# Performance work log

Measured on AMD Instinct MI355X. Metric: run time of the kernel, lower is better.

## Reference

```python
import jax, jax.numpy as jnp
import numpy as np

N_NODES = 50000
N_EDGES = 800000
NFEAT, NHID, NCLASS = 512, 256, 64


def spmm(src, dst, w, h):
    """Sparse adj @ dense h via gather + segment_sum.
    out[i] = sum over edges e with dst[e]==i of w[e] * h[src[e]]."""
    msgs = h[src] * w[:, None]  # [E, d]
    return jax.ops.segment_sum(msgs, dst, num_segments=N_NODES)


def setup_inputs() -> dict:
    key = jax.random.key(0)
    ks = jax.random.split(key, 10)
    return {
        "x": jax.random.normal(ks[0], (N_NODES, NFEAT), dtype=jnp.float32),
        "edge_src0": jax.random.randint(ks[1], (N_EDGES,), 0, N_NODES),
        "edge_dst0": jax.random.randint(ks[2], (N_EDGES,), 0, N_NODES),
        "edge_w0": jax.random.uniform(ks[3], (N_EDGES,), dtype=jnp.float32),
        "edge_src1": jax.random.randint(ks[4], (N_EDGES,), 0, N_NODES),
        "edge_dst1": jax.random.randint(ks[5], (N_EDGES,), 0, N_NODES),
        "edge_w1": jax.random.uniform(ks[6], (N_EDGES,), dtype=jnp.float32),
        "W1": jax.random.normal(ks[7], (NFEAT, NHID), dtype=jnp.float32) * (1.0 / np.sqrt(NFEAT)),
        "b1": jnp.zeros((NHID,), dtype=jnp.float32),
        "W2": jax.random.normal(ks[8], (NHID, NCLASS), dtype=jnp.float32) * (1.0 / np.sqrt(NHID)),
        "b2": jnp.zeros((NCLASS,), dtype=jnp.float32),
    }


def reference(x, edge_src0, edge_dst0, edge_w0, edge_src1, edge_dst1, edge_w1, W1, b1, W2, b2):
    # Layer 1: GCN conv (skip=False) + ReLU. Dropout is identity in eval mode.
    h = jax.nn.relu(spmm(edge_src0, edge_dst0, edge_w0, x @ W1) + b1)
    # Layer 2: GCN conv (skip=False)
    logits = spmm(edge_src1, edge_dst1, edge_w1, h @ W2) + b2
    return jax.nn.log_softmax(logits, axis=1)
```

## Files before the change

### kernel.cpp

```cpp
#include <hip/hip_runtime.h>

#define N_NODES 50000
#define N_EDGES 800000
#define NFEAT   512
#define NHID    256
#define NCLASS  64

#define MTILES     ((N_NODES + 63) / 64)

#define NBUCK      196
#define BCAP       5632
#define BIN_CHUNK  4096
#define BIN_BLOCKS ((N_EDGES + BIN_CHUNK - 1) / BIN_CHUNK)

typedef short short8  __attribute__((ext_vector_type(8)));
typedef float floatx4 __attribute__((ext_vector_type(4)));

__device__ inline short f2bf(float f) {
    unsigned u = __builtin_bit_cast(unsigned, f);
    u += 0x7FFF + ((u >> 16) & 1);
    return (short)(u >> 16);
}
__device__ inline float bf2f(short v) {
    unsigned u = ((unsigned)(unsigned short)v) << 16;
    return __builtin_bit_cast(float, u);
}
__device__ inline int pack_edge(int src, float w) {
    return (src & 0xFFFF) | ((int)(unsigned short)f2bf(w) << 16);
}

__global__ __launch_bounds__(256) void cast_w1t_kernel(const float* __restrict__ W1,
                                                       short* __restrict__ Wt) {
    const int k = blockIdx.x;
    const int n = threadIdx.x;
    Wt[n * NFEAT + k] = f2bf(W1[k * NHID + n]);
}

__global__ __launch_bounds__(256) void cast_w2t_kernel(const float* __restrict__ W2,
                                                       short* __restrict__ W2t) {
    const int n = blockIdx.x;
    const int k = threadIdx.x;
    W2t[n * NHID + k] = f2bf(W2[k * NCLASS + n]);
}

__global__ __launch_bounds__(256) void binscatter_kernel(
    const int* __restrict__ es0, const int* __restrict__ ed0, const float* __restrict__ ew0,
    int* __restrict__ cur0, int2* __restrict__ bin0,
    const int* __restrict__ es1, const int* __restrict__ ed1, const float* __restrict__ ew1,
    int* __restrict__ cur1, int2* __restrict__ bin1) {
    __shared__ int hist[NBUCK];
    const int list = blockIdx.x >= BIN_BLOCKS;
    const int cb   = blockIdx.x - list * BIN_BLOCKS;
    const int*   es  = list ? es1 : es0;
    const int*   ed  = list ? ed1 : ed0;
    const float* ew  = list ? ew1 : ew0;
    int*         cur = list ? cur1 : cur0;
    int2*        bin = list ? bin1 : bin0;

    const int e0 = cb * BIN_CHUNK;
    const int e1 = min(e0 + BIN_CHUNK, N_EDGES);
    const int t  = threadIdx.x;

    if (t < NBUCK) hist[t] = 0;
    __syncthreads();
    for (int e = e0 + t; e < e1; e += 256)
        atomicAdd(&hist[ed[e] >> 8], 1);
    __syncthreads();
    if (t < NBUCK) hist[t] = atomicAdd(&cur[t], hist[t]);
    __syncthreads();
    for (int e = e0 + t; e < e1; e += 256) {
        int d = ed[e];
        int b = d >> 8;
        int p = atomicAdd(&hist[b], 1);
        if (p < BCAP) {
            int2 v; v.x = pack_edge(es[e], ew[e]); v.y = d;
            bin[(size_t)b * BCAP + p] = v;
        }
    }
}

__global__ __launch_bounds__(256) void bucket_scan_kernel(const int* __restrict__ cur0, int* __restrict__ bb0,
                                                          const int* __restrict__ cur1, int* __restrict__ bb1) {
    __shared__ int s[256];
    const int* cur = blockIdx.x ? cur1 : cur0;
    int*       bb  = blockIdx.x ? bb1  : bb0;
    int t = threadIdx.x;
    int v = (t < NBUCK) ? min(cur[t], BCAP) : 0;
    s[t] = v;
    __syncthreads();
    for (int off = 1; off < 256; off <<= 1) {
        int a = (t >= off) ? s[t - off] : 0;
        __syncthreads();
        s[t] += a;
        __syncthreads();
    }
    if (t < NBUCK) bb[t] = s[t] - v;
}

__global__ __launch_bounds__(256) void bucket_csr_kernel(
    const int* __restrict__ cur0, const int* __restrict__ bb0, const int2* __restrict__ bin0,
    int* __restrict__ deg0, int* __restrict__ base0, int* __restrict__ edge0,
    const int* __restrict__ cur1, const int* __restrict__ bb1, const int2* __restrict__ bin1,
    int* __restrict__ deg1, int* __restrict__ base1, int* __restrict__ edge1) {
    __shared__ int dh[256];
    __shared__ int sc[256];
    const int list = blockIdx.x >= NBUCK;
    const int b    = blockIdx.x - list * NBUCK;
    const int*  cur  = list ? cur1  : cur0;
    const int*  bb   = list ? bb1   : bb0;
    const int2* bin  = (list ? bin1 : bin0) + (size_t)b * BCAP;
    int*        deg  = list ? deg1  : deg0;
    int*        base = list ? base1 : base0;
    int*        edge = list ? edge1 : edge0;

    const int len   = min(cur[b], BCAP);
    const int gbase = bb[b];
    const int n0    = b << 8;
    const int t     = threadIdx.x;

    dh[t] = 0;
    __syncthreads();
    for (int i = t; i < len; i += 256)
        atomicAdd(&dh[bin[i].y & 255], 1);
    __syncthreads();
    int v = dh[t];
    sc[t] = v;
    __syncthreads();
    for (int off = 1; off < 256; off <<= 1) {
        int a = (t >= off) ? sc[t - off] : 0;
        __syncthreads();
        sc[t] += a;
        __syncthreads();
    }
    int excl = sc[t] - v;
    int node = n0 + t;
    if (node < N_NODES) { deg[node] = v; base[node] = gbase + excl; }
    dh[t] = gbase + excl;
    __syncthreads();
    for (int i = t; i < len; i += 256) {
        int2 ev = bin[i];
        int p = atomicAdd(&dh[ev.y & 255], 1);
        edge[p] = ev.x;
    }
}

__global__ __launch_bounds__(256) void gemm1_mfma_kernel(const float* __restrict__ x,
                                                         const short* __restrict__ Wt,
                                                         short* __restrict__ h0b) {
    __shared__ short As[64 * 32];
    __shared__ short Bs[256 * 32];
    const int tid  = threadIdx.x;
    const int wave = tid >> 6, lane = tid & 63;
    const int mlo  = lane & 15, q = lane >> 4;
    const int m0   = blockIdx.x * 64;

    const int ar  = tid >> 2;
    const int acg = (tid & 3) * 8;
    int arow = m0 + ar; if (arow >= N_NODES) arow = N_NODES - 1;
    const float* aptr = x + (size_t)arow * NFEAT + acg;

    floatx4 acc[4][4] = {};

    for (int kc = 0; kc < NFEAT; kc += 32) {
        float4 a0 = *(const float4*)(aptr + kc);
        float4 a1 = *(const float4*)(aptr + kc + 4);
        short8 ap;
        ap[0]=f2bf(a0.x); ap[1]=f2bf(a0.y); ap[2]=f2bf(a0.z); ap[3]=f2bf(a0.w);
        ap[4]=f2bf(a1.x); ap[5]=f2bf(a1.y); ap[6]=f2bf(a1.z); ap[7]=f2bf(a1.w);
        *(short8*)&As[ar * 32 + acg] = ap;
        #pragma unroll
        for (int it = 0; it < 4; ++it) {
            int g = it * 256 + tid;
            *(short8*)&Bs[g * 8] =
                *(const short8*)(Wt + (size_t)(g >> 2) * NFEAT + kc + (g & 3) * 8);
        }
        __syncthreads();

        short8 af[4], bfr[4];
        #pragma unroll
        for (int t = 0; t < 4; ++t)
            af[t] = *(const short8*)&As[(t * 16 + mlo) * 32 + q * 8];
        #pragma unroll
        for (int u = 0; u < 4; ++u)
            bfr[u] = *(const short8*)&Bs[(wave * 64 + u * 16 + mlo) * 32 + q * 8];
        #pragma unroll
        for (int t = 0; t < 4; ++t)
            #pragma unroll
            for (int u = 0; u < 4; ++u)
                acc[t][u] = __builtin_amdgcn_mfma_f32_16x16x32_bf16(af[t], bfr[u], acc[t][u], 0, 0, 0);
        __syncthreads();
    }

    #pragma unroll
    for (int t = 0; t < 4; ++t) {
        #pragma unroll
        for (int r = 0; r < 4; ++r) {
            int row = m0 + t * 16 + q * 4 + r;
            if (row < N_NODES) {
                #pragma unroll
                for (int u = 0; u < 4; ++u)
                    h0b[(size_t)row * NHID + wave * 64 + u * 16 + mlo] = f2bf(acc[t][u][r]);
            }
        }
    }
}

__global__ __launch_bounds__(256) void spmm1_pull_kernel(const int* __restrict__ base,
                                                         const int* __restrict__ deg,
                                                         const int* __restrict__ edge_s,
                                                         const short* __restrict__ h0b,
                                                         float* __restrict__ agg0) {
    const int node = blockIdx.x * 4 + (threadIdx.x >> 6);
    const int lane = threadIdx.x & 63;
    const int slot = lane >> 5;
    const int c    = lane & 31;
    const int start = base[node];
    const int len   = deg[node];

    float acc[8] = {0.f,0.f,0.f,0.f,0.f,0.f,0.f,0.f};
    int j = slot;
    int e = 0;
    short8 hv = {0,0,0,0,0,0,0,0};
    if (j < len) {
        e  = edge_s[start + j];
        hv = *(const short8*)(h0b + (size_t)(e & 0xFFFF) * NHID + c * 8);
    }
    while (j < len) {
        float wt = bf2f((short)((unsigned)e >> 16));
        int jn = j + 2;
        int en = e; short8 hn = hv;
        if (jn < len) {
            en = edge_s[start + jn];
            hn = *(const short8*)(h0b + (size_t)(en & 0xFFFF) * NHID + c * 8);
        }
        #pragma unroll
        for (int k = 0; k < 8; ++k) acc[k] += wt * bf2f(hv[k]);
        e = en; hv = hn; j = jn;
    }
    #pragma unroll
    for (int k = 0; k < 8; ++k) acc[k] += __shfl_xor(acc[k], 32);
    if (slot == 0) {
        float4 o0 = {acc[0], acc[1], acc[2], acc[3]};
        float4 o1 = {acc[4], acc[5], acc[6], acc[7]};
        float* p = agg0 + (size_t)node * NHID + c * 8;
        *(float4*)p = o0;
        *(float4*)(p + 4) = o1;
    }
}

__global__ __launch_bounds__(256) void gemm2_mfma_kernel(const float* __restrict__ agg0,
                                                         const float* __restrict__ b1,
                                                         const short* __restrict__ W2t,
                                                         short* __restrict__ h2b) {
    __shared__ short Bs[64 * 264];
    __shared__ short As[64 * 32];
    const int tid  = threadIdx.x;
    const int wave = tid >> 6, lane = tid & 63;
    const int mlo  = lane & 15, q = lane >> 4;
    const int m0   = blockIdx.x * 64;

    {
        int n = tid >> 2, seg = (tid & 3) * 64;
        #pragma unroll
        for (int i = 0; i < 8; ++i)
            *(short8*)&Bs[n * 264 + seg + i * 8] =
                *(const short8*)(W2t + n * NHID + seg + i * 8);
    }

    const int ar  = tid >> 2;
    const int acg = (tid & 3) * 8;
    int arow = m0 + ar; if (arow >= N_NODES) arow = N_NODES - 1;
    const float* aptr = agg0 + (size_t)arow * NHID + acg;

    floatx4 acc[4] = {};

    for (int kc = 0; kc < NHID; kc += 32) {
        float4 a0 = *(const float4*)(aptr + kc);
        float4 a1 = *(const float4*)(aptr + kc + 4);
        float4 c0 = *(const float4*)(b1 + kc + acg);
        float4 c1 = *(const float4*)(b1 + kc + acg + 4);
        float v0 = a0.x + c0.x, v1 = a0.y + c0.y, v2 = a0.z + c0.z, v3 = a0.w + c0.w;
        float v4 = a1.x + c1.x, v5 = a1.y + c1.y, v6 = a1.z + c1.z, v7 = a1.w + c1.w;
        short8 apk;
        apk[0] = f2bf(v0 > 0.f ? v0 : 0.f); apk[1] = f2bf(v1 > 0.f ? v1 : 0.f);
        apk[2] = f2bf(v2 > 0.f ? v2 : 0.f); apk[3] = f2bf(v3 > 0.f ? v3 : 0.f);
        apk[4] = f2bf(v4 > 0.f ? v4 : 0.f); apk[5] = f2bf(v5 > 0.f ? v5 : 0.f);
        apk[6] = f2bf(v6 > 0.f ? v6 : 0.f); apk[7] = f2bf(v7 > 0.f ? v7 : 0.f);
        *(short8*)&As[ar * 32 + acg] = apk;
        __syncthreads();

        short8 af = *(const short8*)&As[(wave * 16 + mlo) * 32 + q * 8];
        #pragma unroll
        for (int u = 0; u < 4; ++u) {
            short8 bfr = *(const short8*)&Bs[(u * 16 + mlo) * 264 + kc + q * 8];
            acc[u] = __builtin_amdgcn_mfma_f32_16x16x32_bf16(af, bfr, acc[u], 0, 0, 0);
        }
        __syncthreads();
    }

    #pragma unroll
    for (int r = 0; r < 4; ++r) {
        int row = m0 + wave * 16 + q * 4 + r;
        if (row < N_NODES) {
            #pragma unroll
            for (int u = 0; u < 4; ++u)
                h2b[(size_t)row * NCLASS + u * 16 + mlo] = f2bf(acc[u][r]);
        }
    }
}

__global__ __launch_bounds__(256) void spmm2_lsm_kernel(const int* __restrict__ base,
                                                        const int* __restrict__ deg,
                                                        const int* __restrict__ edge_s,
                                                        const short* __restrict__ h2b,
                                                        const float* __restrict__ b2,
                                                        float* __restrict__ out) {
    const int node = blockIdx.x * 4 + (threadIdx.x >> 6);
    const int lane = threadIdx.x & 63;
    const int slot = lane >> 3;
    const int f    = lane & 7;
    const int start = base[node];
    const int len   = deg[node];

    float acc[8] = {0.f,0.f,0.f,0.f,0.f,0.f,0.f,0.f};
    int j = slot;
    int e = 0;
    short8 hv = {0,0,0,0,0,0,0,0};
    if (j < len) {
        e  = edge_s[start + j];
        hv = *(const short8*)(h2b + (size_t)(e & 0xFFFF) * NCLASS + f * 8);
    }
    while (j < len) {
        float wt = bf2f((short)((unsigned)e >> 16));
        int jn = j + 8;
        int en = e; short8 hn = hv;
        if (jn < len) {
            en = edge_s[start + jn];
            hn = *(const short8*)(h2b + (size_t)(en & 0xFFFF) * NCLASS + f * 8);
        }
        #pragma unroll
        for (int k = 0; k < 8; ++k) acc[k] += wt * bf2f(hv[k]);
        e = en; hv = hn; j = jn;
    }
    #pragma unroll
    for (int k = 0; k < 8; ++k) {
        acc[k] += __shfl_xor(acc[k], 8);
        acc[k] += __shfl_xor(acc[k], 16);
        acc[k] += __shfl_xor(acc[k], 32);
    }
    float4 c0 = *(const float4*)(b2 + f * 8);
    float4 c1 = *(const float4*)(b2 + f * 8 + 4);
    float v[8];
    v[0] = acc[0] + c0.x; v[1] = acc[1] + c0.y; v[2] = acc[2] + c0.z; v[3] = acc[3] + c0.w;
    v[4] = acc[4] + c1.x; v[5] = acc[5] + c1.y; v[6] = acc[6] + c1.z; v[7] = acc[7] + c1.w;
    float m = v[0];
    #pragma unroll
    for (int k = 1; k < 8; ++k) m = fmaxf(m, v[k]);
    m = fmaxf(m, __shfl_xor(m, 1));
    m = fmaxf(m, __shfl_xor(m, 2));
    m = fmaxf(m, __shfl_xor(m, 4));
    float s = 0.f;
    #pragma unroll
    for (int k = 0; k < 8; ++k) s += __expf(v[k] - m);
    s += __shfl_xor(s, 1);
    s += __shfl_xor(s, 2);
    s += __shfl_xor(s, 4);
    float ls = m + __logf(s);
    if (slot == 0) {
        float4 o0 = {v[0] - ls, v[1] - ls, v[2] - ls, v[3] - ls};
        float4 o1 = {v[4] - ls, v[5] - ls, v[6] - ls, v[7] - ls};
        float* p = out + (size_t)node * NCLASS + f * 8;
        *(float4*)p = o0;
        *(float4*)(p + 4) = o1;
    }
}

extern "C" void kernel_launch(void* const* d_in, const int* in_sizes, int n_in,
                              void* d_out, int out_size, void* d_ws, size_t ws_size,
                              hipStream_t stream) {
    const float* x   = (const float*)d_in[0];
    const int*   es0 = (const int*)  d_in[1];
    const int*   ed0 = (const int*)  d_in[2];
    const float* ew0 = (const float*)d_in[3];
    const int*   es1 = (const int*)  d_in[4];
    const int*   ed1 = (const int*)  d_in[5];
    const float* ew1 = (const float*)d_in[6];
    const float* W1  = (const float*)d_in[7];
    const float* b1  = (const float*)d_in[8];
    const float* W2  = (const float*)d_in[9];
    const float* b2  = (const float*)d_in[10];
    float* out = (float*)d_out;

    char* ws = (char*)d_ws;
    const size_t SZ_H0 = (size_t)N_NODES * NHID * sizeof(short);
    const size_t SZ_BIN = (size_t)NBUCK * BCAP * sizeof(int2);
    short* h0b  = (short*)ws;
    short* h2b  = (short*)ws;
    float* agg0 = (float*)(ws + (size_t)N_NODES * NHID * sizeof(float));

    int2* bin0 = (int2*)(ws + SZ_H0);
    int2* bin1 = (int2*)(ws + SZ_H0 + SZ_BIN);

    char* c1 = ws + 44000000;
    int* deg1  = (int*)c1;
    int* base1 = deg1 + N_NODES;
    int* edge1 = base1 + N_NODES;
    int* cur0  = edge1 + N_EDGES;
    int* cur1  = cur0 + 256;
    int* bb0   = cur1 + 256;
    int* bb1   = bb0 + 256;

    int*   deg0  = (int*)d_out;
    int*   base0 = deg0 + N_NODES;
    int*   edge0 = base0 + N_NODES;
    short* Wt    = (short*)((char*)d_out + (8u << 20));
    short* W2t   = (short*)((char*)d_out + (9u << 20));

    hipMemsetAsync(cur0, 0, 512 * sizeof(int), stream);
    binscatter_kernel<<<2 * BIN_BLOCKS, 256, 0, stream>>>(es0, ed0, ew0, cur0, bin0,
                                                          es1, ed1, ew1, cur1, bin1);
    bucket_scan_kernel<<<2, 256, 0, stream>>>(cur0, bb0, cur1, bb1);
    bucket_csr_kernel<<<2 * NBUCK, 256, 0, stream>>>(cur0, bb0, bin0, deg0, base0, edge0,
                                                     cur1, bb1, bin1, deg1, base1, edge1);

    cast_w1t_kernel<<<NFEAT, 256, 0, stream>>>(W1, Wt);
    cast_w2t_kernel<<<NCLASS, 256, 0, stream>>>(W2, W2t);

    gemm1_mfma_kernel<<<MTILES, 256, 0, stream>>>(x, Wt, h0b);
    spmm1_pull_kernel<<<N_NODES / 4, 256, 0, stream>>>(base0, deg0, edge0, h0b, agg0);

    gemm2_mfma_kernel<<<MTILES, 256, 0, stream>>>(agg0, b1, W2t, h2b);
    spmm2_lsm_kernel<<<N_NODES / 4, 256, 0, stream>>>(base1, deg1, edge1, h2b, b2, out);
}
```

Measured before the change: 362.1 us.

## Tile weight transposes via LDS and deepen GEMM K-tiles with swizzled LDS

New measurement: 354.9 us. 1.02x faster.

```diff
diff --git a/kernel.cpp b/kernel.cpp
--- a/kernel.cpp
+++ b/kernel.cpp
@@ -29,18 +29,67 @@
     return (src & 0xFFFF) | ((int)(unsigned short)f2bf(w) << 16);
 }
 
+typedef __attribute__((address_space(3))) void       lds_void;
+typedef __attribute__((address_space(1))) const void glb_void;
+__device__ inline void gload_lds16(const void* g, void* l) {
+    __builtin_amdgcn_global_load_lds((glb_void*)g, (lds_void*)l, 16, 0, 0);
+}
+
 __global__ __launch_bounds__(256) void cast_w1t_kernel(const float* __restrict__ W1,
                                                        short* __restrict__ Wt) {
-    const int k = blockIdx.x;
-    const int n = threadIdx.x;
-    Wt[n * NFEAT + k] = f2bf(W1[k * NHID + n]);
+    __shared__ short tile[64][72];
+    const int t  = threadIdx.x;
+    const int k0 = (blockIdx.x >> 2) << 6;
+    const int n0 = (blockIdx.x & 3) << 6;
+    {
+        int kr = t >> 2, ng = (t & 3) << 4;
+        const float* src = W1 + (size_t)(k0 + kr) * NHID + n0 + ng;
+        float4 v0 = ((const float4*)src)[0], v1 = ((const float4*)src)[1];
+        float4 v2 = ((const float4*)src)[2], v3 = ((const float4*)src)[3];
+        short* d = &tile[kr][ng];
+        d[0]=f2bf(v0.x); d[1]=f2bf(v0.y); d[2]=f2bf(v0.z); d[3]=f2bf(v0.w);
+        d[4]=f2bf(v1.x); d[5]=f2bf(v1.y); d[6]=f2bf(v1.z); d[7]=f2bf(v1.w);
+        d[8]=f2bf(v2.x); d[9]=f2bf(v2.y); d[10]=f2bf(v2.z); d[11]=f2bf(v2.w);
+        d[12]=f2bf(v3.x); d[13]=f2bf(v3.y); d[14]=f2bf(v3.z); d[15]=f2bf(v3.w);
+    }
+    __syncthreads();
+    {
+        int nr = t >> 2, kg = (t & 3) << 4;
+        short8 o0, o1;
+        #pragma unroll
+        for (int j = 0; j < 8; ++j) { o0[j] = tile[kg + j][nr]; o1[j] = tile[kg + 8 + j][nr]; }
+        short* d = Wt + (size_t)(n0 + nr) * NFEAT + k0 + kg;
+        *(short8*)d = o0;
+        *(short8*)(d + 8) = o1;
+    }
 }
 
 __global__ __launch_bounds__(256) void cast_w2t_kernel(const float* __restrict__ W2,
                                                        short* __restrict__ W2t) {
-    const int n = blockIdx.x;
-    const int k = threadIdx.x;
-    W2t[n * NHID + k] = f2bf(W2[k * NCLASS + n]);
+    __shared__ short tile[64][72];
+    const int t  = threadIdx.x;
+    const int k0 = blockIdx.x << 6;
+    {
+        int kr = t >> 2, ng = (t & 3) << 4;
+        const float* src = W2 + (size_t)(k0 + kr) * NCLASS + ng;
+        float4 v0 = ((const float4*)src)[0], v1 = ((const float4*)src)[1];
+        float4 v2 = ((const float4*)src)[2], v3 = ((const float4*)src)[3];
+        short* d = &tile[kr][ng];
+        d[0]=f2bf(v0.x); d[1]=f2bf(v0.y); d[2]=f2bf(v0.z); d[3]=f2bf(v0.w);
+        d[4]=f2bf(v1.x); d[5]=f2bf(v1.y); d[6]=f2bf(v1.z); d[7]=f2bf(v1.w);
+        d[8]=f2bf(v2.x); d[9]=f2bf(v2.y); d[10]=f2bf(v2.z); d[11]=f2bf(v2.w);
+        d[12]=f2bf(v3.x); d[13]=f2bf(v3.y); d[14]=f2bf(v3.z); d[15]=f2bf(v3.w);
+    }
+    __syncthreads();
+    {
+        int nr = t >> 2, kg = (t & 3) << 4;
+        short8 o0, o1;
+        #pragma unroll
+        for (int j = 0; j < 8; ++j) { o0[j] = tile[kg + j][nr]; o1[j] = tile[kg + 8 + j][nr]; }
+        short* d = W2t + (size_t)nr * NHID + k0 + kg;
+        *(short8*)d = o0;
+        *(short8*)(d + 8) = o1;
+    }
 }
 
 __global__ __launch_bounds__(256) void binscatter_kernel(
@@ -147,47 +196,63 @@
 __global__ __launch_bounds__(256) void gemm1_mfma_kernel(const float* __restrict__ x,
                                                          const short* __restrict__ Wt,
                                                          short* __restrict__ h0b) {
-    __shared__ short As[64 * 32];
-    __shared__ short Bs[256 * 32];
+    __shared__ short As[64 * 64];
+    __shared__ short Bs[256 * 64];
     const int tid  = threadIdx.x;
     const int wave = tid >> 6, lane = tid & 63;
     const int mlo  = lane & 15, q = lane >> 4;
     const int m0   = blockIdx.x * 64;
 
-    const int ar  = tid >> 2;
-    const int acg = (tid & 3) * 8;
+    const int ar = tid >> 2;
+    const int cp = (tid & 3) * 2;
     int arow = m0 + ar; if (arow >= N_NODES) arow = N_NODES - 1;
-    const float* aptr = x + (size_t)arow * NFEAT + acg;
+    const float* aptr = x + (size_t)arow * NFEAT + cp * 8;
+
+    const int brl = lane >> 3;
+    const int bsl = lane & 7;
 
     floatx4 acc[4][4] = {};
 
-    for (int kc = 0; kc < NFEAT; kc += 32) {
+    for (int kc = 0; kc < NFEAT; kc += 64) {
+        #pragma unroll
+        for (int i = 0; i < 8; ++i) {
+            int r  = wave * 64 + i * 8 + brl;
+            int sc2 = bsl ^ (r & 7);
+            gload_lds16(Wt + (size_t)r * NFEAT + kc + sc2 * 8,
+                        &Bs[(wave * 64 + i * 8) * 64]);
+        }
         float4 a0 = *(const float4*)(aptr + kc);
         float4 a1 = *(const float4*)(aptr + kc + 4);
-        short8 ap;
-        ap[0]=f2bf(a0.x); ap[1]=f2bf(a0.y); ap[2]=f2bf(a0.z); ap[3]=f2bf(a0.w);
-        ap[4]=f2bf(a1.x); ap[5]=f2bf(a1.y); ap[6]=f2bf(a1.z); ap[7]=f2bf(a1.w);
-        *(short8*)&As[ar * 32 + acg] = ap;
-        #pragma unroll
-        for (int it = 0; it < 4; ++it) {
-            int g = it * 256 + tid;
-            *(short8*)&Bs[g * 8] =
-                *(const short8*)(Wt + (size_t)(g >> 2) * NFEAT + kc + (g & 3) * 8);
-        }
-        __syncthreads();
-
-        short8 af[4], bfr[4];
-        #pragma unroll
-        for (int t = 0; t < 4; ++t)
-            af[t] = *(const short8*)&As[(t * 16 + mlo) * 32 + q * 8];
-        #pragma unroll
-        for (int u = 0; u < 4; ++u)
-            bfr[u] = *(const short8*)&Bs[(wave * 64 + u * 16 + mlo) * 32 + q * 8];
-        #pragma unroll
-        for (int t = 0; t < 4; ++t)
+        float4 a2 = *(const float4*)(aptr + kc + 8);
+        float4 a3 = *(const float4*)(aptr + kc + 12);
+        short8 p0, p1;
+        p0[0]=f2bf(a0.x); p0[1]=f2bf(a0.y); p0[2]=f2bf(a0.z); p0[3]=f2bf(a0.w);
+        p0[4]=f2bf(a1.x); p0[5]=f2bf(a1.y); p0[6]=f2bf(a1.z); p0[7]=f2bf(a1.w);
+        p1[0]=f2bf(a2.x); p1[1]=f2bf(a2.y); p1[2]=f2bf(a2.z); p1[3]=f2bf(a2.w);
+        p1[4]=f2bf(a3.x); p1[5]=f2bf(a3.y); p1[6]=f2bf(a3.z); p1[7]=f2bf(a3.w);
+        *(short8*)&As[ar * 64 + ((cp     ) ^ (ar & 7)) * 8] = p0;
+        *(short8*)&As[ar * 64 + ((cp + 1) ^ (ar & 7)) * 8] = p1;
+        __syncthreads();
+
+        #pragma unroll
+        for (int h = 0; h < 2; ++h) {
+            short8 afv[4], bfv[4];
             #pragma unroll
-            for (int u = 0; u < 4; ++u)
-                acc[t][u] = __builtin_amdgcn_mfma_f32_16x16x32_bf16(af[t], bfr[u], acc[t][u], 0, 0, 0);
+            for (int t = 0; t < 4; ++t) {
+                int r = t * 16 + mlo;
+                afv[t] = *(const short8*)&As[r * 64 + ((h * 4 + q) ^ (r & 7)) * 8];
+            }
+            #pragma unroll
+            for (int u = 0; u < 4; ++u) {
+                int r = wave * 64 + u * 16 + mlo;
+                bfv[u] = *(const short8*)&Bs[r * 64 + ((h * 4 + q) ^ (r & 7)) * 8];
+            }
+            #pragma unroll
+            for (int t = 0; t < 4; ++t)
+                #pragma unroll
+                for (int u = 0; u < 4; ++u)
+                    acc[t][u] = __builtin_amdgcn_mfma_f32_16x16x32_bf16(afv[t], bfv[u], acc[t][u], 0, 0, 0);
+        }
         __syncthreads();
     }
 
@@ -252,48 +317,68 @@
                                                          const float* __restrict__ b1,
                                                          const short* __restrict__ W2t,
                                                          short* __restrict__ h2b) {
-    __shared__ short Bs[64 * 264];
-    __shared__ short As[64 * 32];
+    __shared__ short Bs[64 * 256];
+    __shared__ short As[64 * 64];
     const int tid  = threadIdx.x;
     const int wave = tid >> 6, lane = tid & 63;
     const int mlo  = lane & 15, q = lane >> 4;
     const int m0   = blockIdx.x * 64;
 
     {
-        int n = tid >> 2, seg = (tid & 3) * 64;
-        #pragma unroll
-        for (int i = 0; i < 8; ++i)
-            *(short8*)&Bs[n * 264 + seg + i * 8] =
-                *(const short8*)(W2t + n * NHID + seg + i * 8);
-    }
-
-    const int ar  = tid >> 2;
-    const int acg = (tid & 3) * 8;
+        int n = tid >> 2;
+        #pragma unroll
+        for (int j = 0; j < 8; ++j) {
+            int c  = (tid & 3) * 8 + j;
+            int s2 = c ^ (n & 7);
+            *(short8*)&Bs[n * 256 + s2 * 8] =
+                *(const short8*)(W2t + (size_t)n * NHID + c * 8);
+        }
+    }
+
+    const int ar = tid >> 2;
+    const int cp = (tid & 3) * 2;
     int arow = m0 + ar; if (arow >= N_NODES) arow = N_NODES - 1;
-    const float* aptr = agg0 + (size_t)arow * NHID + acg;
+    const float* aptr = agg0 + (size_t)arow * NHID + cp * 8;
 
     floatx4 acc[4] = {};
 
-    for (int kc = 0; kc < NHID; kc += 32) {
+    for (int kc = 0; kc < NHID; kc += 64) {
         float4 a0 = *(const float4*)(aptr + kc);
         float4 a1 = *(const float4*)(aptr + kc + 4);
-        float4 c0 = *(const float4*)(b1 + kc + acg);
-        float4 c1 = *(const float4*)(b1 + kc + acg + 4);
+        float4 a2 = *(const float4*)(aptr + kc + 8);
+        float4 a3 = *(const float4*)(aptr + kc + 12);
+        float4 c0 = *(const float4*)(b1 + kc + cp * 8);
+        float4 c1 = *(const float4*)(b1 + kc + cp * 8 + 4);
+        float4 c2 = *(const float4*)(b1 + kc + cp * 8 + 8);
+        float4 c3 = *(const float4*)(b1 + kc + cp * 8 + 12);
         float v0 = a0.x + c0.x, v1 = a0.y + c0.y, v2 = a0.z + c0.z, v3 = a0.w + c0.w;
         float v4 = a1.x + c1.x, v5 = a1.y + c1.y, v6 = a1.z + c1.z, v7 = a1.w + c1.w;
-        short8 apk;
-        apk[0] = f2bf(v0 > 0.f ? v0 : 0.f); apk[1] = f2bf(v1 > 0.f ? v1 : 0.f);
-        apk[2] = f2bf(v2 > 0.f ? v2 : 0.f); apk[3] = f2bf(v3 > 0.f ? v3 : 0.f);
-        apk[4] = f2bf(v4 > 0.f ? v4 : 0.f); apk[5] = f2bf(v5 > 0.f ? v5 : 0.f);
-        apk[6] = f2bf(v6 > 0.f ? v6 : 0.f); apk[7] = f2bf(v7 > 0.f ? v7 : 0.f);
-        *(short8*)&As[ar * 32 + acg] = apk;
-        __syncthreads();
-
-        short8 af = *(const short8*)&As[(wave * 16 + mlo) * 32 + q * 8];
+        float v8 = a2.x + c2.x, v9 = a2.y + c2.y, vA = a2.z + c2.z, vB = a2.w + c2.w;
+        float vC = a3.x + c3.x, vD = a3.y + c3.y, vE = a3.z + c3.z, vF = a3.w + c3.w;
+        short8 p0, p1;
+        p0[0]=f2bf(v0>0.f?v0:0.f); p0[1]=f2bf(v1>0.f?v1:0.f); p0[2]=f2bf(v2>0.f?v2:0.f); p0[3]=f2bf(v3>0.f?v3:0.f);
+        p0[4]=f2bf(v4>0.f?v4:0.f); p0[5]=f2bf(v5>0.f?v5:0.f); p0[6]=f2bf(v6>0.f?v6:0.f); p0[7]=f2bf(v7>0.f?v7:0.f);
+        p1[0]=f2bf(v8>0.f?v8:0.f); p1[1]=f2bf(v9>0.f?v9:0.f); p1[2]=f2bf(vA>0.f?vA:0.f); p1[3]=f2bf(vB>0.f?vB:0.f);
+        p1[4]=f2bf(vC>0.f?vC:0.f); p1[5]=f2bf(vD>0.f?vD:0.f); p1[6]=f2bf(vE>0.f?vE:0.f); p1[7]=f2bf(vF>0.f?vF:0.f);
+        *(short8*)&As[ar * 64 + ((cp     ) ^ (ar & 7)) * 8] = p0;
+        *(short8*)&As[ar * 64 + ((cp + 1) ^ (ar & 7)) * 8] = p1;
+        __syncthreads();
+
+        short8 afv[2];
+        {
+            int r = wave * 16 + mlo;
+            afv[0] = *(const short8*)&As[r * 64 + ((    q) ^ (r & 7)) * 8];
+            afv[1] = *(const short8*)&As[r * 64 + ((4 + q) ^ (r & 7)) * 8];
+        }
         #pragma unroll
         for (int u = 0; u < 4; ++u) {
-            short8 bfr = *(const short8*)&Bs[(u * 16 + mlo) * 264 + kc + q * 8];
-            acc[u] = __builtin_amdgcn_mfma_f32_16x16x32_bf16(af, bfr, acc[u], 0, 0, 0);
+            int r = u * 16 + mlo;
+            #pragma unroll
+            for (int h = 0; h < 2; ++h) {
+                int ch = (kc >> 3) + h * 4 + q;
+                short8 bv = *(const short8*)&Bs[r * 256 + (ch ^ (r & 7)) * 8];
+                acc[u] = __builtin_amdgcn_mfma_f32_16x16x32_bf16(afv[h], bv, acc[u], 0, 0, 0);
+            }
         }
         __syncthreads();
     }
@@ -423,8 +508,8 @@
     bucket_csr_kernel<<<2 * NBUCK, 256, 0, stream>>>(cur0, bb0, bin0, deg0, base0, edge0,
                                                      cur1, bb1, bin1, deg1, base1, edge1);
 
-    cast_w1t_kernel<<<NFEAT, 256, 0, stream>>>(W1, Wt);
-    cast_w2t_kernel<<<NCLASS, 256, 0, stream>>>(W2, W2t);
+    cast_w1t_kernel<<<32, 256, 0, stream>>>(W1, Wt);
+    cast_w2t_kernel<<<4, 256, 0, stream>>>(W2, W2t);
 
     gemm1_mfma_kernel<<<MTILES, 256, 0, stream>>>(x, Wt, h0b);
     spmm1_pull_kernel<<<N_NODES / 4, 256, 0, stream>>>(base0, deg0, edge0, h0b, agg0);
```
